# Performance work log

Measured on AMD Instinct MI355X. Metric: run time of the kernel, lower is better.

The kernel has to match this reference:

```python
import jax, jax.numpy as jnp
import numpy as np

FEATURE_DIM = 4
H_PATCHES = 16
W_PATCHES = 16
PATCH_H = 16
PATCH_W = 16
D = FEATURE_DIM * PATCH_H * PATCH_W  # 1024
N = 2 * H_PATCHES * W_PATCHES        # 512
M = 256
B = 64
EPS = 1e-5


def layernorm(x, g, b):
    mu = jnp.mean(x, axis=-1, keepdims=True)
    var = jnp.var(x, axis=-1, keepdims=True)
    return (x - mu) * jax.lax.rsqrt(var + EPS) * g + b


def box3x3(x):
    # per-channel 3x3 window sum with zero padding == diagonal conv in BCIM
    p = jnp.pad(x, ((0, 0), (0, 0), (1, 1), (1, 1)))
    H, W = x.shape[2], x.shape[3]
    return sum(p[:, :, i:i + H, j:j + W] for i in range(3) for j in range(3))


def setup_inputs() -> dict:
    key = jax.random.key(0)
    ks = jax.random.split(key, 20)
    rn = lambda k, shp, s=0.02: (jax.random.normal(k, shp, dtype=jnp.float32) * s)
    inp = {
        'p_vector': jax.random.normal(ks[0], (B, N, D), dtype=jnp.float32),
        'object_vector': jax.random.normal(ks[1], (M, D), dtype=jnp.float32),
        'ln_p_g': 1.0 + rn(ks[2], (D,), 0.1), 'ln_p_b': rn(ks[3], (D,)),
        'ln_o_g': 1.0 + rn(ks[4], (D,), 0.1), 'ln_o_b': rn(ks[5], (D,)),
        'Wq': rn(ks[6], (D, D)), 'bq': rn(ks[7], (D,)),
        'Wk': rn(ks[8], (D, D)), 'bk': rn(ks[9], (D,)),
        'Wv': rn(ks[10], (D, D)), 'bv': rn(ks[11], (D,)),
        'W1': rn(ks[12], (D, D)), 'b1': rn(ks[13], (D,)),
        'ln1_g': 1.0 + rn(ks[14], (D,), 0.1), 'ln1_b': rn(ks[15], (D,)),
        'W2': rn(ks[16], (D, D)), 'b2': rn(ks[17], (D,)),
        'ln2_g': 1.0 + rn(ks[18], (D,), 0.1), 'ln2_b': rn(ks[19], (D,)),
    }
    return inp


def reference(p_vector, object_vector, ln_p_g, ln_p_b, ln_o_g, ln_o_b,
              Wq, bq, Wk, bk, Wv, bv, W1, b1, ln1_g, ln1_b,
              W2, b2, ln2_g, ln2_b):
    # cross-attention (single head, full D)
    p = layernorm(p_vector, ln_p_g, ln_p_b)            # [B,N,D]
    o = layernorm(object_vector, ln_o_g, ln_o_b)       # [M,D]
    q = jnp.einsum('bnd,de->bne', p, Wq) + bq
    k = o @ Wk + bk                                    # [M,D]
    v = o @ Wv + bv
    A = jax.nn.softmax(jnp.einsum('bnd,md->bnm', q, k), axis=-1)
    p = p + jnp.einsum('bnm,md->bnd', A, v)
    # projection block: Linear->LN->GELU->Linear->LN->GELU, residual
    h = jax.nn.gelu(layernorm(jnp.einsum('bnd,de->bne', p, W1) + b1, ln1_g, ln1_b), approximate=False)
    h = jax.nn.gelu(layernorm(jnp.einsum('bnd,de->bne', h, W2) + b2, ln2_g, ln2_b), approximate=False)
    p = p + h
    # BCIM: reshape to image of 2D channels
    x = jnp.transpose(p, (0, 2, 1)).reshape(B, 2 * D, H_PATCHES, W_PATCHES)
    norm = jnp.linalg.norm(x, axis=1, keepdims=True)
    unit = x / norm
    win = box3x3(unit) / 9.0
    sim = jnp.sum(unit * win, axis=1, keepdims=True)   # [B,1,hp,wp]
    x = x * sim
    # reshape back to [B, 2*hp*wp, D]
    x = jnp.transpose(x, (0, 2, 3, 1)).reshape(B, H_PATCHES, W_PATCHES, D, 2)
    x = jnp.transpose(x, (0, 4, 1, 2, 3)).reshape(B, 2 * H_PATCHES * W_PATCHES, D)
    return x
```

## Files before the change

### kernel.cpp

```cpp
#include <hip/hip_runtime.h>
#include <math.h>

#define D_DIM 1024
#define M_DIM 256
#define B_IMG 64
#define N_TOK 512
#define BN    32768

typedef unsigned short u16;
typedef __attribute__((ext_vector_type(8))) __bf16 bf16x8;
typedef __attribute__((ext_vector_type(4))) float  f32x4;

__device__ __forceinline__ u16 f2bf(float f) {
  union { float f; unsigned u; } c; c.f = f;
  unsigned u = c.u;
  return (u16)((u + 0x7FFFu + ((u >> 16) & 1u)) >> 16);
}
__device__ __forceinline__ float bf2f(u16 h) {
  union { unsigned u; float f; } c; c.u = ((unsigned)h) << 16;
  return c.f;
}

__global__ __launch_bounds__(64) void detect_dtype(const u16* __restrict__ p, int* __restrict__ dflag)
{
  const int lane = threadIdx.x;
  const float a = fabsf(bf2f(p[lane * 2]));
  const bool sane = (a >= 1e-20f && a <= 1e3f);
  const unsigned long long m = __ballot(sane);
  if (lane == 0) *dflag = (m == ~0ull) ? 0 : 1;
}

__device__ __forceinline__ float load_in(const void* p, size_t i, int f) {
  return f ? ((const float*)p)[i] : bf2f(((const u16*)p)[i]);
}

template<int EPI>
__global__ __launch_bounds__(256) void gemm_bt(
    const u16* __restrict__ X0, const u16* __restrict__ X1, const u16* __restrict__ X2,
    const u16* __restrict__ Bt0, const u16* __restrict__ Bt1, const u16* __restrict__ Bt2,
    const void* __restrict__ bias, const int* __restrict__ dflag,
    int np_base, int np_extra,
    const u16* res_hi, const u16* res_lo,
    float* outf, u16* outb, u16* outb2,
    int R, int K, int NC)
{
  __shared__ u16 lA[128 * 64];
  __shared__ u16 lB[128 * 64];
  const int tid  = threadIdx.x;
  const int wave = tid >> 6, lane = tid & 63;
  const int quad = lane >> 4, l15 = lane & 15;
  const int wr = wave & 1, wc = wave >> 1;
  const int rblk = blockIdx.x, cblk = blockIdx.y;

  const int np = np_base + (np_extra ? np_extra * (*dflag) : 0);

  const int srow = lane >> 3;
  const int scol = ((lane & 7) ^ (srow & 7)) * 8;

  const u16* Xs[3] = {X0, X1, X2};
  const u16* Bs[3] = {Bt0, Bt1, Bt2};

  f32x4 acc[4][4] = {};

  for (int p = 0; p < np; ++p) {
    const u16* gA = Xs[p] + (size_t)(rblk * 128 + srow) * K + scol;
    const u16* gB = Bs[p] + (size_t)(cblk * 128 + srow) * K + scol;
    for (int k0 = 0; k0 < K; k0 += 64) {
#pragma unroll
      for (int i = 0; i < 4; ++i) {
        const int j = i * 4 + wave;
        __builtin_amdgcn_global_load_lds(
            (const __attribute__((address_space(1))) void*)(gA + (size_t)j * 8 * K + k0),
            (__attribute__((address_space(3))) void*)(lA + j * 512), 16, 0, 0);
        __builtin_amdgcn_global_load_lds(
            (const __attribute__((address_space(1))) void*)(gB + (size_t)j * 8 * K + k0),
            (__attribute__((address_space(3))) void*)(lB + j * 512), 16, 0, 0);
      }
      __syncthreads();
#pragma unroll
      for (int s = 0; s < 2; ++s) {
        bf16x8 af[4], bfr[4];
#pragma unroll
        for (int r = 0; r < 4; ++r) {
          const int row  = wr * 64 + r * 16 + l15;
          const int slot = (s * 4 + quad) ^ (row & 7);
          af[r] = *(const bf16x8*)(lA + row * 64 + slot * 8);
        }
#pragma unroll
        for (int c = 0; c < 4; ++c) {
          const int row  = wc * 64 + c * 16 + l15;
          const int slot = (s * 4 + quad) ^ (row & 7);
          bfr[c] = *(const bf16x8*)(lB + row * 64 + slot * 8);
        }
#pragma unroll
        for (int r = 0; r < 4; ++r)
#pragma unroll
          for (int c = 0; c < 4; ++c)
            acc[r][c] = __builtin_amdgcn_mfma_f32_16x16x32_bf16(af[r], bfr[c], acc[r][c], 0, 0, 0);
      }
      __syncthreads();
    }
  }

  const int fdt = bias ? *dflag : 0;
  const int crow0 = rblk * 128 + wr * 64;
  const int ccol0 = cblk * 128 + wc * 64;
#pragma unroll
  for (int c = 0; c < 4; ++c) {
    const int col = ccol0 + c * 16 + l15;
    const float bcol = bias ? load_in(bias, col, fdt) : 0.0f;
#pragma unroll
    for (int r = 0; r < 4; ++r) {
#pragma unroll
      for (int t = 0; t < 4; ++t) {
        const int row = crow0 + r * 16 + quad * 4 + t;
        const size_t idx = (size_t)row * NC + col;
        float v = acc[r][c][t] + bcol;
        if (EPI == 0) {
          outb[idx] = f2bf(v);
        } else if (EPI == 1) {
          outf[idx] = v;
        } else if (EPI == 2) {
          const float p = bf2f(res_hi[idx]) + bf2f(res_lo[idx]) + v;
          const u16 hi = f2bf(p);
          outb[idx]  = hi;
          outb2[idx] = f2bf(p - bf2f(hi));
        } else if (EPI == 3) {
          outb[(size_t)col * R + row] = f2bf(v);
        } else {
          const u16 hi = f2bf(v);
          outb[idx]  = hi;
          outb2[idx] = f2bf(v - bf2f(hi));
        }
      }
    }
  }
}

template<int EPI>
__global__ __launch_bounds__(512, 2) void gemm256(
    const u16* __restrict__ X0, const u16* __restrict__ X1, const u16* __restrict__ X2,
    const u16* __restrict__ Bt0, const u16* __restrict__ Bt1, const u16* __restrict__ Bt2,
    const void* __restrict__ bias, const int* __restrict__ dflag,
    int np_base, int np_extra,
    const u16* res_hi, const u16* res_lo,
    float* outf, u16* outb, u16* outb2,
    int R, int K, int NC)
{
  extern __shared__ u16 lds2[];
  const int tid  = threadIdx.x;
  const int wave = tid >> 6, lane = tid & 63;
  const int quad = lane >> 4, l15 = lane & 15;
  const int wm = wave >> 2, wn = wave & 3;
  const int rblk = blockIdx.x, cblk = blockIdx.y;

  const int np = np_base + (np_extra ? np_extra * (*dflag) : 0);
  const int ktiles = K >> 6;
  const int ktl = 31 - __builtin_clz(ktiles);
  const int NT = np << ktl;

  const u16* Xs[3] = {X0, X1, X2};
  const u16* Bs[3] = {Bt0, Bt1, Bt2};

  const int srow = lane >> 3;
  const int scol = ((lane & 7) ^ srow) * 8;

  f32x4 acc[8][4] = {};

  auto stage = [&](int t) {
    const int p  = t >> ktl;
    const int k0 = (t & (ktiles - 1)) << 6;
    const u16* gA = Xs[p] + (size_t)(rblk * 256 + srow) * K + k0 + scol;
    const u16* gB = Bs[p] + (size_t)(cblk * 256 + srow) * K + k0 + scol;
    u16* dst = lds2 + (t & 1) * 32768;
#pragma unroll
    for (int i = 0; i < 4; ++i) {
      const int r0 = i * 64 + wave * 8;
      __builtin_amdgcn_global_load_lds(
          (const __attribute__((address_space(1))) void*)(gA + (size_t)r0 * K),
          (__attribute__((address_space(3))) void*)(dst + r0 * 64), 16, 0, 0);
      __builtin_amdgcn_global_load_lds(
          (const __attribute__((address_space(1))) void*)(gB + (size_t)r0 * K),
          (__attribute__((address_space(3))) void*)(dst + 16384 + r0 * 64), 16, 0, 0);
    }
  };

  stage(0);
  stage(1);
  asm volatile("s_waitcnt vmcnt(8)" ::: "memory");
  asm volatile("s_barrier" ::: "memory");

  for (int t = 0; t < NT; ++t) {
    const u16* bufA = lds2 + (t & 1) * 32768;
    const u16* bufB = bufA + 16384;
    __builtin_amdgcn_s_setprio(1);
#pragma unroll
    for (int kk = 0; kk < 2; ++kk) {
      bf16x8 bfr[4];
#pragma unroll
      for (int n = 0; n < 4; ++n) {
        const int row  = wn * 64 + n * 16 + l15;
        const int slot = (kk * 4 + quad) ^ (row & 7);
        bfr[n] = *(const bf16x8*)(bufB + row * 64 + slot * 8);
      }
#pragma unroll
      for (int m = 0; m < 8; ++m) {
        const int row  = wm * 128 + m * 16 + l15;
        const int slot = (kk * 4 + quad) ^ (row & 7);
        const bf16x8 a = *(const bf16x8*)(bufA + row * 64 + slot * 8);
#pragma unroll
        for (int n = 0; n < 4; ++n)
          acc[m][n] = __builtin_amdgcn_mfma_f32_16x16x32_bf16(a, bfr[n], acc[m][n], 0, 0, 0);
      }
    }
    __builtin_amdgcn_s_setprio(0);
    asm volatile("s_barrier" ::: "memory");
    if (t + 2 < NT) {
      stage(t + 2);
      asm volatile("s_waitcnt vmcnt(8)" ::: "memory");
      asm volatile("s_barrier" ::: "memory");
    } else if (t + 1 < NT) {
      asm volatile("s_waitcnt vmcnt(0)" ::: "memory");
      asm volatile("s_barrier" ::: "memory");
    }
  }

  const int fdt = bias ? *dflag : 0;
  const int crow0 = rblk * 256 + wm * 128;
  const int ccol0 = cblk * 256 + wn * 64;
#pragma unroll
  for (int n = 0; n < 4; ++n) {
    const int col = ccol0 + n * 16 + l15;
    const float bcol = bias ? load_in(bias, col, fdt) : 0.0f;
#pragma unroll
    for (int m = 0; m < 8; ++m) {
#pragma unroll
      for (int u = 0; u < 4; ++u) {
        const int row = crow0 + m * 16 + quad * 4 + u;
        const size_t idx = (size_t)row * NC + col;
        float v = acc[m][n][u] + bcol;
        if (EPI == 0) {
          outb[idx] = f2bf(v);
        } else if (EPI == 1) {
          outf[idx] = v;
        } else if (EPI == 2) {
          const float pp = bf2f(res_hi[idx]) + bf2f(res_lo[idx]) + v;
          const u16 hi = f2bf(pp);
          outb[idx]  = hi;
          outb2[idx] = f2bf(pp - bf2f(hi));
        } else {
          const u16 hi = f2bf(v);
          outb[idx]  = hi;
          outb2[idx] = f2bf(v - bf2f(hi));
        }
      }
    }
  }
}

__global__ __launch_bounds__(256) void ln_row(
    const void* __restrict__ x, const void* __restrict__ g, const void* __restrict__ b,
    const int* __restrict__ dflag, u16* __restrict__ oh, u16* __restrict__ ol)
{
  const int f = *dflag;
  const int row = blockIdx.x, tid = threadIdx.x;
  const int col = tid * 4;
  const size_t base = (size_t)row * 1024 + col;
  float v0, v1, v2, v3;
  if (f) {
    const float4 xv = *(const float4*)((const float*)x + base);
    v0 = xv.x; v1 = xv.y; v2 = xv.z; v3 = xv.w;
  } else {
    const ushort4 xv = *(const ushort4*)((const u16*)x + base);
    v0 = bf2f(xv.x); v1 = bf2f(xv.y); v2 = bf2f(xv.z); v3 = bf2f(xv.w);
  }
  float s  = v0 + v1 + v2 + v3;
  float sq = v0 * v0 + v1 * v1 + v2 * v2 + v3 * v3;
#pragma unroll
  for (int o = 32; o > 0; o >>= 1) { s += __shfl_xor(s, o); sq += __shfl_xor(sq, o); }
  __shared__ float red[8];
  if ((tid & 63) == 0) { red[tid >> 6] = s; red[4 + (tid >> 6)] = sq; }
  __syncthreads();
  s  = red[0] + red[1] + red[2] + red[3];
  sq = red[4] + red[5] + red[6] + red[7];
  const float mean = s * (1.0f / 1024.0f);
  const float var  = sq * (1.0f / 1024.0f) - mean * mean;
  const float rs   = rsqrtf(var + 1e-5f);
  float y[4];
  y[0] = (v0 - mean) * rs * load_in(g, col + 0, f) + load_in(b, col + 0, f);
  y[1] = (v1 - mean) * rs * load_in(g, col + 1, f) + load_in(b, col + 1, f);
  y[2] = (v2 - mean) * rs * load_in(g, col + 2, f) + load_in(b, col + 2, f);
  y[3] = (v3 - mean) * rs * load_in(g, col + 3, f) + load_in(b, col + 3, f);
  ushort4 hv, lv;
  hv.x = f2bf(y[0]); lv.x = f2bf(y[0] - bf2f(hv.x));
  hv.y = f2bf(y[1]); lv.y = f2bf(y[1] - bf2f(hv.y));
  hv.z = f2bf(y[2]); lv.z = f2bf(y[2] - bf2f(hv.z));
  hv.w = f2bf(y[3]); lv.w = f2bf(y[3] - bf2f(hv.w));
  *(ushort4*)(oh + base) = hv;
  *(ushort4*)(ol + base) = lv;
}

template<int MODE>
__global__ __launch_bounds__(256) void ln_gelu(
    const u16* __restrict__ x, const void* __restrict__ g, const void* __restrict__ b,
    const int* __restrict__ dflag,
    const u16* res_hi, const u16* res_lo,
    u16* ob, u16* oh, u16* ol)
{
  const int f = *dflag;
  const int row = blockIdx.x, tid = threadIdx.x;
  const int col = tid * 4;
  const size_t base = (size_t)row * 1024 + col;
  const ushort4 xv = *(const ushort4*)(x + base);
  const float v0 = bf2f(xv.x), v1 = bf2f(xv.y), v2 = bf2f(xv.z), v3 = bf2f(xv.w);
  float s  = v0 + v1 + v2 + v3;
  float sq = v0 * v0 + v1 * v1 + v2 * v2 + v3 * v3;
#pragma unroll
  for (int o = 32; o > 0; o >>= 1) { s += __shfl_xor(s, o); sq += __shfl_xor(sq, o); }
  __shared__ float red[8];
  if ((tid & 63) == 0) { red[tid >> 6] = s; red[4 + (tid >> 6)] = sq; }
  __syncthreads();
  s  = red[0] + red[1] + red[2] + red[3];
  sq = red[4] + red[5] + red[6] + red[7];
  const float mean = s * (1.0f / 1024.0f);
  const float var  = sq * (1.0f / 1024.0f) - mean * mean;
  const float rs   = rsqrtf(var + 1e-5f);
  float z[4], h[4];
  z[0] = (v0 - mean) * rs * load_in(g, col + 0, f) + load_in(b, col + 0, f);
  z[1] = (v1 - mean) * rs * load_in(g, col + 1, f) + load_in(b, col + 1, f);
  z[2] = (v2 - mean) * rs * load_in(g, col + 2, f) + load_in(b, col + 2, f);
  z[3] = (v3 - mean) * rs * load_in(g, col + 3, f) + load_in(b, col + 3, f);
#pragma unroll
  for (int i = 0; i < 4; ++i)
    h[i] = 0.5f * z[i] * (1.0f + erff(z[i] * 0.70710678118654752f));
  if (MODE == 0) {
    *(ushort4*)(ob + base) = make_ushort4(f2bf(h[0]), f2bf(h[1]), f2bf(h[2]), f2bf(h[3]));
  } else {
    const ushort4 rh = *(const ushort4*)(res_hi + base);
    const ushort4 rl = *(const ushort4*)(res_lo + base);
    float p[4];
    p[0] = bf2f(rh.x) + bf2f(rl.x) + h[0];
    p[1] = bf2f(rh.y) + bf2f(rl.y) + h[1];
    p[2] = bf2f(rh.z) + bf2f(rl.z) + h[2];
    p[3] = bf2f(rh.w) + bf2f(rl.w) + h[3];
    ushort4 hv, lv;
    hv.x = f2bf(p[0]); lv.x = f2bf(p[0] - bf2f(hv.x));
    hv.y = f2bf(p[1]); lv.y = f2bf(p[1] - bf2f(hv.y));
    hv.z = f2bf(p[2]); lv.z = f2bf(p[2] - bf2f(hv.z));
    hv.w = f2bf(p[3]); lv.w = f2bf(p[3] - bf2f(hv.w));
    *(ushort4*)(oh + base) = hv;
    *(ushort4*)(ol + base) = lv;
  }
}

__global__ __launch_bounds__(256) void softmax256(const float* __restrict__ S, u16* __restrict__ A)
{
  const int tid = threadIdx.x, lane = tid & 63, wave = tid >> 6;
  const size_t row = (size_t)blockIdx.x * 4 + wave;
  const float4 v = *(const float4*)(S + row * 256 + lane * 4);
  float m = fmaxf(fmaxf(v.x, v.y), fmaxf(v.z, v.w));
#pragma unroll
  for (int o = 32; o > 0; o >>= 1) m = fmaxf(m, __shfl_xor(m, o));
  const float e0 = expf(v.x - m), e1 = expf(v.y - m), e2 = expf(v.z - m), e3 = expf(v.w - m);
  float s = e0 + e1 + e2 + e3;
#pragma unroll
  for (int o = 32; o > 0; o >>= 1) s += __shfl_xor(s, o);
  const float r = 1.0f / s;
  *(ushort4*)(A + row * 256 + lane * 4) =
      make_ushort4(f2bf(e0 * r), f2bf(e1 * r), f2bf(e2 * r), f2bf(e3 * r));
}

__global__ __launch_bounds__(256) void wtrans5(
    const void* w0, const void* w1, const void* w2, const void* w3, const void* w4,
    u16* h0, u16* h1, u16* h2, u16* h3, u16* h4,
    u16* l0, u16* l1, u16* l2, u16* l3, u16* l4,
    const int* __restrict__ dflag)
{
  const int f = *dflag;
  const void* W; u16* H; u16* L;
  switch (blockIdx.z) {
    case 0: W = w0; H = h0; L = l0; break;
    case 1: W = w1; H = h1; L = l1; break;
    case 2: W = w2; H = h2; L = l2; break;
    case 3: W = w3; H = h3; L = l3; break;
    default: W = w4; H = h4; L = l4; break;
  }
  __shared__ u16 th[32][33];
  __shared__ u16 tl[32][33];
  const int tx = threadIdx.x & 31, ty = threadIdx.x >> 5;
  const int bx = blockIdx.x, by = blockIdx.y;
#pragma unroll
  for (int i = 0; i < 4; ++i) {
    const int r = ty + i * 8;
    const float v = load_in(W, ((size_t)by * 32 + r) * 1024 + bx * 32 + tx, f);
    const u16 hi = f2bf(v);
    th[r][tx] = hi;
    tl[r][tx] = f2bf(v - bf2f(hi));
  }
  __syncthreads();
#pragma unroll
  for (int i = 0; i < 4; ++i) {
    const int r = ty + i * 8;
    const size_t o = ((size_t)bx * 32 + r) * 1024 + by * 32 + tx;
    H[o] = th[tx][r];
    L[o] = tl[tx][r];
  }
}

__global__ __launch_bounds__(256) void zerof(float* p, int n)
{
  const int i = blockIdx.x * 256 + threadIdx.x;
  if (i < n) p[i] = 0.0f;
}

__global__ __launch_bounds__(256) void bcim_dots(
    const u16* __restrict__ p2h, const u16* __restrict__ p2l, float* __restrict__ G)
{
  const int b = blockIdx.x, ds = blockIdx.y;
  __shared__ float T[512][17];
  float acc[9] = {0, 0, 0, 0, 0, 0, 0, 0, 0};
  const int tid = threadIdx.x;
  const int px = tid & 15, py = tid >> 4;
  for (int ch = 0; ch < 8; ++ch) {
    const int d0 = ds * 128 + ch * 16;
#pragma unroll
    for (int i = 0; i < 8; ++i) {
      const int j = i * 256 + tid;
      const int r = j >> 2, q4 = j & 3;
      const size_t base = ((size_t)b * 512 + r) * 1024 + d0 + q4 * 4;
      const ushort4 hv = *(const ushort4*)(p2h + base);
      const ushort4 lv = *(const ushort4*)(p2l + base);
      T[r][q4 * 4 + 0] = bf2f(hv.x) + bf2f(lv.x);
      T[r][q4 * 4 + 1] = bf2f(hv.y) + bf2f(lv.y);
      T[r][q4 * 4 + 2] = bf2f(hv.z) + bf2f(lv.z);
      T[r][q4 * 4 + 3] = bf2f(hv.w) + bf2f(lv.w);
    }
    __syncthreads();
    float a0[16], a1[16];
#pragma unroll
    for (int dc = 0; dc < 16; ++dc) { a0[dc] = T[tid][dc]; a1[dc] = T[tid + 256][dc]; }
#pragma unroll
    for (int o = 0; o < 9; ++o) {
      const int dy = o / 3 - 1, dx = o % 3 - 1;
      const int qx = px + dx, qy = py + dy;
      if (qx >= 0 && qx < 16 && qy >= 0 && qy < 16) {
        const int qp = qy * 16 + qx;
        float sum = 0.0f;
#pragma unroll
        for (int dc = 0; dc < 16; ++dc)
          sum += a0[dc] * T[qp][dc] + a1[dc] * T[qp + 256][dc];
        acc[o] += sum;
      }
    }
    __syncthreads();
  }
#pragma unroll
  for (int o = 0; o < 9; ++o)
    atomicAdd(&G[((size_t)b * 9 + o) * 256 + tid], acc[o]);
}

__global__ __launch_bounds__(256) void bcim_sim_k(const float* __restrict__ G, float* __restrict__ sim)
{
  const int b = blockIdx.x, tid = threadIdx.x;
  __shared__ float nrm[256];
  const float nv = sqrtf(G[((size_t)b * 9 + 4) * 256 + tid]);
  nrm[tid] = nv;
  __syncthreads();
  const int px = tid & 15, py = tid >> 4;
  float s = 0.0f;
#pragma unroll
  for (int o = 0; o < 9; ++o) {
    const int dy = o / 3 - 1, dx = o % 3 - 1;
    const int qx = px + dx, qy = py + dy;
    if (qx >= 0 && qx < 16 && qy >= 0 && qy < 16)
      s += G[((size_t)b * 9 + o) * 256 + tid] / (nv * nrm[qy * 16 + qx]);
  }
  sim[b * 256 + tid] = s * (1.0f / 9.0f);
}

__global__ __launch_bounds__(256) void bcim_scale(
    const u16* __restrict__ p2h, const u16* __restrict__ p2l,
    const float* __restrict__ sim, float* __restrict__ out)
{
  const size_t i4 = (size_t)blockIdx.x * 256 + threadIdx.x;
  const size_t base = i4 * 4;
  const ushort4 hv = *(const ushort4*)(p2h + base);
  const ushort4 lv = *(const ushort4*)(p2l + base);
  const size_t n = base >> 10;
  const size_t b = n >> 9;
  const int pix = (int)(n & 255);
  const float s = sim[b * 256 + pix];
  *(float4*)(out + base) = make_float4(
      (bf2f(hv.x) + bf2f(lv.x)) * s, (bf2f(hv.y) + bf2f(lv.y)) * s,
      (bf2f(hv.z) + bf2f(lv.z)) * s, (bf2f(hv.w) + bf2f(lv.w)) * s);
}

extern "C" void kernel_launch(void* const* d_in, const int* in_sizes, int n_in,
                              void* d_out, int out_size, void* d_ws, size_t ws_size,
                              hipStream_t stream)
{
  (void)in_sizes; (void)n_in; (void)out_size; (void)ws_size;
  const void* p_vector      = d_in[0];
  const void* object_vector = d_in[1];
  const void* ln_p_g = d_in[2];
  const void* ln_p_b = d_in[3];
  const void* ln_o_g = d_in[4];
  const void* ln_o_b = d_in[5];
  const void* Wq = d_in[6];  const void* bq = d_in[7];
  const void* Wk = d_in[8];  const void* bk = d_in[9];
  const void* Wv = d_in[10]; const void* bv = d_in[11];
  const void* W1 = d_in[12]; const void* b1 = d_in[13];
  const void* ln1_g = d_in[14]; const void* ln1_b = d_in[15];
  const void* W2 = d_in[16]; const void* b2 = d_in[17];
  const void* ln2_g = d_in[18]; const void* ln2_b = d_in[19];
  float* out = (float*)d_out;

  char* ws = (char*)d_ws;
  size_t off = 0;
  auto alloc = [&](size_t bytes) -> void* {
    void* p = ws + off;
    off += (bytes + 255) & ~(size_t)255;
    return p;
  };
  int* dflag = (int*)alloc(256);
  u16* WqH = (u16*)alloc((size_t)D_DIM * D_DIM * 2);
  u16* WkH = (u16*)alloc((size_t)D_DIM * D_DIM * 2);
  u16* WvH = (u16*)alloc((size_t)D_DIM * D_DIM * 2);
  u16* W1H = (u16*)alloc((size_t)D_DIM * D_DIM * 2);
  u16* W2H = (u16*)alloc((size_t)D_DIM * D_DIM * 2);
  u16* WqL = (u16*)alloc((size_t)D_DIM * D_DIM * 2);
  u16* WkL = (u16*)alloc((size_t)D_DIM * D_DIM * 2);
  u16* WvL = (u16*)alloc((size_t)D_DIM * D_DIM * 2);
  u16* W1L = (u16*)alloc((size_t)D_DIM * D_DIM * 2);
  u16* W2L = (u16*)alloc((size_t)D_DIM * D_DIM * 2);
  u16* PH = (u16*)alloc((size_t)BN * D_DIM * 2);
  u16* PL = (u16*)alloc((size_t)BN * D_DIM * 2);
  u16* QH = (u16*)alloc((size_t)BN * D_DIM * 2);
  u16* QL = (u16*)alloc((size_t)BN * D_DIM * 2);
  float* S_f = (float*)alloc((size_t)BN * M_DIM * 4);
  u16* A_b   = (u16*)alloc((size_t)BN * M_DIM * 2);
  u16* onH = (u16*)alloc((size_t)M_DIM * D_DIM * 2);
  u16* onL = (u16*)alloc((size_t)M_DIM * D_DIM * 2);
  u16* kH  = (u16*)alloc((size_t)M_DIM * D_DIM * 2);
  u16* kL  = (u16*)alloc((size_t)M_DIM * D_DIM * 2);
  u16* vT  = (u16*)alloc((size_t)D_DIM * M_DIM * 2);
  float* G   = (float*)alloc((size_t)B_IMG * 9 * 256 * 4);
  float* sim = (float*)alloc((size_t)B_IMG * 256 * 4);

  detect_dtype<<<1, 64, 0, stream>>>((const u16*)p_vector, dflag);
  wtrans5<<<dim3(32, 32, 5), 256, 0, stream>>>(Wq, Wk, Wv, W1, W2,
      WqH, WkH, WvH, W1H, W2H, WqL, WkL, WvL, W1L, W2L, dflag);
  zerof<<<(B_IMG * 9 * 256 + 255) / 256, 256, 0, stream>>>(G, B_IMG * 9 * 256);

  ln_row<<<BN, 256, 0, stream>>>(p_vector, ln_p_g, ln_p_b, dflag, PH, PL);
  ln_row<<<M_DIM, 256, 0, stream>>>(object_vector, ln_o_g, ln_o_b, dflag, onH, onL);

  gemm_bt<4><<<dim3(2, 8), 256, 0, stream>>>(onH, onL, onH, WkH, WkH, WkL,
      bk, dflag, 2, 1, nullptr, nullptr, nullptr, kH, kL, M_DIM, D_DIM, D_DIM);
  gemm_bt<3><<<dim3(2, 8), 256, 0, stream>>>(onH, onL, onH, WvH, WvH, WvL,
      bv, dflag, 2, 1, nullptr, nullptr, nullptr, vT, nullptr, M_DIM, D_DIM, D_DIM);
  gemm256<4><<<dim3(128, 4), 512, 131072, stream>>>(PH, PL, PH, WqH, WqH, WqL,
      bq, dflag, 2, 1, nullptr, nullptr, nullptr, QH, QL, BN, D_DIM, D_DIM);

  gemm256<1><<<dim3(128, 1), 512, 131072, stream>>>(QH, QL, QH, kH, kH, kL,
      nullptr, dflag, 3, 0, nullptr, nullptr, S_f, nullptr, nullptr, BN, D_DIM, M_DIM);
  softmax256<<<BN / 4, 256, 0, stream>>>(S_f, A_b);

  gemm256<2><<<dim3(128, 4), 512, 131072, stream>>>(A_b, nullptr, nullptr, vT, nullptr, nullptr,
      nullptr, dflag, 1, 0, PH, PL, nullptr, PH, PL, BN, M_DIM, D_DIM);

  gemm256<0><<<dim3(128, 4), 512, 131072, stream>>>(PH, nullptr, nullptr, W1H, nullptr, nullptr,
      b1, dflag, 1, 0, nullptr, nullptr, nullptr, QH, nullptr, BN, D_DIM, D_DIM);
  ln_gelu<0><<<BN, 256, 0, stream>>>(QH, ln1_g, ln1_b, dflag, nullptr, nullptr, QL, nullptr, nullptr);

  gemm256<0><<<dim3(128, 4), 512, 131072, stream>>>(QL, nullptr, nullptr, W2H, nullptr, nullptr,
      b2, dflag, 1, 0, nullptr, nullptr, nullptr, QH, nullptr, BN, D_DIM, D_DIM);
  ln_gelu<1><<<BN, 256, 0, stream>>>(QH, ln2_g, ln2_b, dflag, PH, PL, nullptr, PH, PL);

  bcim_dots<<<dim3(B_IMG, 8), 256, 0, stream>>>(PH, PL, G);
  bcim_sim_k<<<B_IMG, 256, 0, stream>>>(G, sim);
  bcim_scale<<<(BN * D_DIM / 4) / 256, 256, 0, stream>>>(PH, PL, sim, out);
}
```

Baseline: 1.566 ms.

## Restructure gemm256 into a 4-buffer BK=32 pipeline with split MFMA phases

The 256x256 GEMM main loop now uses 32-wide K tiles in a four-slot LDS ring. Prefetch is issued two tiles ahead and interleaved between two half-tile MFMA phases, with a new XOR swizzle and barrier/waitcnt placement meant to overlap global loads, LDS reads and MFMA. The QK^T score GEMM also moves from gemm256 to the smaller gemm_bt kernel to get more blocks for the narrow N=256 output. This brings more barriers per K step and a clamped redundant tail load, and the shared memory launch size stays at 128KB though the ring only uses 128KB worth of slots.

```diff
diff --git a/kernel.cpp b/kernel.cpp
--- a/kernel.cpp
+++ b/kernel.cpp
@@ -155,74 +155,92 @@
   const int rblk = blockIdx.x, cblk = blockIdx.y;
 
   const int np = np_base + (np_extra ? np_extra * (*dflag) : 0);
-  const int ktiles = K >> 6;
+  const int ktiles = K >> 5;
   const int ktl = 31 - __builtin_clz(ktiles);
   const int NT = np << ktl;
 
   const u16* Xs[3] = {X0, X1, X2};
   const u16* Bs[3] = {Bt0, Bt1, Bt2};
 
-  const int srow = lane >> 3;
-  const int scol = ((lane & 7) ^ srow) * 8;
+  const int srow  = lane >> 2;
+  const int sslot = lane & 3;
 
   f32x4 acc[8][4] = {};
 
-  auto stage = [&](int t) {
-    const int p  = t >> ktl;
-    const int k0 = (t & (ktiles - 1)) << 6;
-    const u16* gA = Xs[p] + (size_t)(rblk * 256 + srow) * K + k0 + scol;
-    const u16* gB = Bs[p] + (size_t)(cblk * 256 + srow) * K + k0 + scol;
-    u16* dst = lds2 + (t & 1) * 32768;
-#pragma unroll
-    for (int i = 0; i < 4; ++i) {
-      const int r0 = i * 64 + wave * 8;
+  auto stage_tile = [&](int t) {
+    const int tc = t < NT ? t : NT - 1;
+    const int p  = tc >> ktl;
+    const int k0 = (tc & (ktiles - 1)) << 5;
+    u16* dst = lds2 + (t & 3) * 16384;
+#pragma unroll
+    for (int i = 0; i < 2; ++i) {
+      const int rbase = wave * 32 + i * 16;
+      const int r  = rbase + srow;
+      const int cg = (sslot ^ ((r >> 1) & 3)) * 8;
       __builtin_amdgcn_global_load_lds(
-          (const __attribute__((address_space(1))) void*)(gA + (size_t)r0 * K),
-          (__attribute__((address_space(3))) void*)(dst + r0 * 64), 16, 0, 0);
+          (const __attribute__((address_space(1))) void*)(Xs[p] + (size_t)(rblk * 256 + r) * K + k0 + cg),
+          (__attribute__((address_space(3))) void*)(dst + rbase * 32), 16, 0, 0);
+    }
+#pragma unroll
+    for (int i = 0; i < 2; ++i) {
+      const int rbase = wave * 32 + i * 16;
+      const int r  = rbase + srow;
+      const int cg = (sslot ^ ((r >> 1) & 3)) * 8;
       __builtin_amdgcn_global_load_lds(
-          (const __attribute__((address_space(1))) void*)(gB + (size_t)r0 * K),
-          (__attribute__((address_space(3))) void*)(dst + 16384 + r0 * 64), 16, 0, 0);
+          (const __attribute__((address_space(1))) void*)(Bs[p] + (size_t)(cblk * 256 + r) * K + k0 + cg),
+          (__attribute__((address_space(3))) void*)(dst + 8192 + rbase * 32), 16, 0, 0);
     }
   };
 
-  stage(0);
-  stage(1);
-  asm volatile("s_waitcnt vmcnt(8)" ::: "memory");
-  asm volatile("s_barrier" ::: "memory");
+  stage_tile(0);
+  stage_tile(1);
+  asm volatile("s_waitcnt vmcnt(4)" ::: "memory");
+  __builtin_amdgcn_s_barrier();
 
   for (int t = 0; t < NT; ++t) {
-    const u16* bufA = lds2 + (t & 1) * 32768;
-    const u16* bufB = bufA + 16384;
+    const u16* bufA = lds2 + (t & 3) * 16384;
+    const u16* bufB = bufA + 8192;
+    bf16x8 bfr[4], af[4];
+#pragma unroll
+    for (int n = 0; n < 4; ++n) {
+      const int row = wn * 64 + n * 16 + l15;
+      const int ps  = quad ^ ((row >> 1) & 3);
+      bfr[n] = *(const bf16x8*)(bufB + row * 32 + ps * 8);
+    }
+#pragma unroll
+    for (int m = 0; m < 4; ++m) {
+      const int row = wm * 128 + m * 16 + l15;
+      const int ps  = quad ^ ((row >> 1) & 3);
+      af[m] = *(const bf16x8*)(bufA + row * 32 + ps * 8);
+    }
+    stage_tile(t + 2);
+    __builtin_amdgcn_s_barrier();
+    asm volatile("s_waitcnt lgkmcnt(0)" ::: "memory");
     __builtin_amdgcn_s_setprio(1);
 #pragma unroll
-    for (int kk = 0; kk < 2; ++kk) {
-      bf16x8 bfr[4];
-#pragma unroll
-      for (int n = 0; n < 4; ++n) {
-        const int row  = wn * 64 + n * 16 + l15;
-        const int slot = (kk * 4 + quad) ^ (row & 7);
-        bfr[n] = *(const bf16x8*)(bufB + row * 64 + slot * 8);
-      }
-#pragma unroll
-      for (int m = 0; m < 8; ++m) {
-        const int row  = wm * 128 + m * 16 + l15;
-        const int slot = (kk * 4 + quad) ^ (row & 7);
-        const bf16x8 a = *(const bf16x8*)(bufA + row * 64 + slot * 8);
-#pragma unroll
-        for (int n = 0; n < 4; ++n)
-          acc[m][n] = __builtin_amdgcn_mfma_f32_16x16x32_bf16(a, bfr[n], acc[m][n], 0, 0, 0);
-      }
-    }
+    for (int m = 0; m < 4; ++m)
+#pragma unroll
+      for (int n = 0; n < 4; ++n)
+        acc[m][n] = __builtin_amdgcn_mfma_f32_16x16x32_bf16(af[m], bfr[n], acc[m][n], 0, 0, 0);
     __builtin_amdgcn_s_setprio(0);
-    asm volatile("s_barrier" ::: "memory");
-    if (t + 2 < NT) {
-      stage(t + 2);
-      asm volatile("s_waitcnt vmcnt(8)" ::: "memory");
-      asm volatile("s_barrier" ::: "memory");
-    } else if (t + 1 < NT) {
-      asm volatile("s_waitcnt vmcnt(0)" ::: "memory");
-      asm volatile("s_barrier" ::: "memory");
-    }
+    __builtin_amdgcn_s_barrier();
+#pragma unroll
+    for (int m = 0; m < 4; ++m) {
+      const int row = wm * 128 + 64 + m * 16 + l15;
+      const int ps  = quad ^ ((row >> 1) & 3);
+      af[m] = *(const bf16x8*)(bufA + row * 32 + ps * 8);
+    }
+    asm volatile("s_waitcnt vmcnt(4)" ::: "memory");
+    __builtin_amdgcn_s_barrier();
+    asm volatile("s_waitcnt lgkmcnt(0)" ::: "memory");
+    __builtin_amdgcn_s_setprio(1);
+#pragma unroll
+    for (int m = 0; m < 4; ++m)
+#pragma unroll
+      for (int n = 0; n < 4; ++n)
+        acc[4 + m][n] = __builtin_amdgcn_mfma_f32_16x16x32_bf16(af[m], bfr[n], acc[4 + m][n], 0, 0, 0);
+    __builtin_amdgcn_s_setprio(0);
+    __builtin_amdgcn_s_barrier();
   }
 
   const int fdt = bias ? *dflag : 0;
@@ -562,7 +580,7 @@
   gemm256<4><<<dim3(128, 4), 512, 131072, stream>>>(PH, PL, PH, WqH, WqH, WqL,
       bq, dflag, 2, 1, nullptr, nullptr, nullptr, QH, QL, BN, D_DIM, D_DIM);
 
-  gemm256<1><<<dim3(128, 1), 512, 131072, stream>>>(QH, QL, QH, kH, kH, kL,
+  gemm_bt<1><<<dim3(256, 2), 256, 0, stream>>>(QH, QL, QH, kH, kH, kL,
       nullptr, dflag, 3, 0, nullptr, nullptr, S_f, nullptr, nullptr, BN, D_DIM, M_DIM);
   softmax256<<<BN / 4, 256, 0, stream>>>(S_f, A_b);
 
```

New measurement: 1.565 ms. Within noise of the previous version (-0.0%).
